# Optimization experiments

Hardware: AMD Instinct MI355X
Metric: run time of the kernel (lower is better)

## Reference

```python
import jax, jax.numpy as jnp
import numpy as np

N = 100000
E = 1600000
R = 4
D_IN = 128
D_H = 128
C = 2


def _rgcn_conv(x, W, src, dst, et):
    """PyG RGCNConv, root_weight=False, bias=False, aggr='mean'.
    x: [N, d_in], W: [R, d_in, d_out]. Per relation: mean over incoming
    edges of that relation of (x[src] @ W_r), summed over relations.
    """
    n, r = x.shape[0], W.shape[0]
    xw = jnp.einsum('ni,rio->rno', x, W)          # [R, N, d_out]
    m = xw[et, src]                               # [E, d_out] per-edge messages
    key = dst * r + et                            # segment per (dst, relation)
    sums = jax.ops.segment_sum(m, key, num_segments=n * r)
    cnt = jax.ops.segment_sum(jnp.ones((m.shape[0],), m.dtype), key, num_segments=n * r)
    mean = sums / jnp.maximum(cnt, 1.0)[:, None]  # [N*R, d_out]
    return mean.reshape(n, r, -1).sum(axis=1)     # sum over relations -> [N, d_out]


def setup_inputs() -> dict:
    key = jax.random.key(0)
    k = jax.random.split(key, 6)
    x = jax.random.normal(k[0], (N, D_IN), dtype=jnp.float32)
    edge_index = jax.random.randint(k[1], (2, E), 0, N, dtype=jnp.int32)
    edge_type = jax.random.randint(k[2], (E,), 0, R, dtype=jnp.int32)
    # Glorot-ish scaled relation weights per layer
    W1 = jax.random.normal(k[3], (R, D_IN, D_H), dtype=jnp.float32) / np.sqrt(D_IN)
    W2 = jax.random.normal(k[4], (R, D_H, D_H), dtype=jnp.float32) / np.sqrt(D_H)
    W3 = jax.random.normal(k[5], (R, D_H, C), dtype=jnp.float32) / np.sqrt(D_H)
    return {"x": x, "edge_index": edge_index, "edge_type": edge_type,
            "W1": W1, "W2": W2, "W3": W3}


def reference(x, edge_index, edge_type, W1, W2, W3):
    src, dst = edge_index[0], edge_index[1]
    # eval mode: dropout is identity
    h = _rgcn_conv(x, W1, src, dst, edge_type)
    h = jnp.tanh(h)
    h = _rgcn_conv(h, W2, src, dst, edge_type)
    h = jnp.tanh(h)
    h = _rgcn_conv(h, W3, src, dst, edge_type)   # [N, C] logits
    return jax.nn.softmax(h, axis=1), h
```

## Files before the change

### kernel.cpp

```cpp
#include <hip/hip_runtime.h>
#include <math.h>

#define N_NODES 100000
#define N_EDGES 1600000
#define RREL 4
#define DDIM 128
#define KDIM 512
#define NKEY 400000

typedef __bf16 bf16x8 __attribute__((ext_vector_type(8)));
typedef float f32x4 __attribute__((ext_vector_type(4)));

__device__ __forceinline__ float bflo(unsigned u){ return __builtin_bit_cast(float, u << 16); }
__device__ __forceinline__ float bfhi(unsigned u){ return __builtin_bit_cast(float, u & 0xffff0000u); }
__device__ __forceinline__ unsigned f2bf(float f){
  unsigned u = __builtin_bit_cast(unsigned, f);
  return (u + 0x7fffu + ((u >> 16) & 1u)) >> 16;
}
__device__ __forceinline__ int iclamp(int v, int lo, int hi){
  return v < lo ? lo : (v > hi ? hi : v);
}


__global__ void hist_kernel(const int* __restrict__ dst, const int* __restrict__ et,
                            int* __restrict__ counts){
  int e = blockIdx.x * 256 + threadIdx.x;
  int key = iclamp(dst[e] * RREL + et[e], 0, NKEY - 1);
  atomicAdd(&counts[key], 1);
}

__global__ void scan_local(const int* __restrict__ in, int* __restrict__ out,
                           int* __restrict__ bsums, int K){
  __shared__ int s[1024];
  int t = threadIdx.x;
  int i = blockIdx.x * 1024 + t;
  int v = (i < K) ? in[i] : 0;
  s[t] = v; __syncthreads();
  for (int off = 1; off < 1024; off <<= 1){
    int x = (t >= off) ? s[t - off] : 0;
    __syncthreads();
    s[t] += x;
    __syncthreads();
  }
  if (i < K) out[i] = s[t] - v;
  if (t == 1023) bsums[blockIdx.x] = s[t];
}

__global__ void scan_sums(int* __restrict__ b, int nb){
  __shared__ int s[1024];
  int t = threadIdx.x;
  int v = (t < nb) ? b[t] : 0;
  s[t] = v; __syncthreads();
  for (int off = 1; off < 1024; off <<= 1){
    int x = (t >= off) ? s[t - off] : 0;
    __syncthreads();
    s[t] += x;
    __syncthreads();
  }
  if (t < nb) b[t] = s[t] - v;
}

__global__ void scan_add(int* __restrict__ out, int* __restrict__ cursor,
                         const int* __restrict__ bsums, int K, int total){
  int t = threadIdx.x;
  int i = blockIdx.x * 1024 + t;
  if (i < K){
    int v = out[i] + bsums[blockIdx.x];
    out[i] = v;
    cursor[i] = v;
  }
  if (i == 0) out[K] = total;
}

__global__ void scatter_kernel(const int* __restrict__ src, const int* __restrict__ dst,
                               const int* __restrict__ et, int* __restrict__ cursor,
                               int* __restrict__ ssrc){
  int e = blockIdx.x * 256 + threadIdx.x;
  int key = iclamp(dst[e] * RREL + et[e], 0, NKEY - 1);
  int p = atomicAdd(&cursor[key], 1);
  p = iclamp(p, 0, N_EDGES - 1);
  ssrc[p] = iclamp(src[e], 0, N_NODES - 1);
}


__global__ void convert_x(const float* __restrict__ x, unsigned* __restrict__ xb){
  int i = blockIdx.x * 256 + threadIdx.x;
  float2 v = *(const float2*)(x + (size_t)i * 2);
  xb[i] = f2bf(v.x) | (f2bf(v.y) << 16);
}


__global__ void transpose_w(const float* __restrict__ W, unsigned short* __restrict__ Bt){
  int idx = blockIdx.x * 256 + threadIdx.x;
  int k = idx >> 7, n = idx & 127;
  Bt[n * KDIM + k] = (unsigned short)f2bf(W[idx]);
}


__global__ __launch_bounds__(256) void fused_layer(const unsigned* __restrict__ hin,
                                                   const int* __restrict__ ssrc,
                                                   const int* __restrict__ offs,
                                                   const __bf16* __restrict__ Bt,
                                                   unsigned short* __restrict__ hout){
  int tid = threadIdx.x;
  int w = tid >> 6, lane = tid & 63;
  int l15 = lane & 15, quad = lane >> 4;
  int n0w = blockIdx.x * 64 + w * 16;
  int n = n0w + l15;
  int valid = (n < N_NODES);

  f32x4 accC[8];
  #pragma unroll
  for (int tc = 0; tc < 8; tc++) accC[tc] = (f32x4){0.f, 0.f, 0.f, 0.f};

  #pragma unroll
  for (int r = 0; r < RREL; r++){
    int ob = valid ? (n * 4 + r) : 0;
    int beg = iclamp(offs[ob], 0, N_EDGES);
    int end = iclamp(offs[ob + 1], beg, N_EDGES);
    if (!valid){ beg = 0; end = 0; }

    float ac[32];
    #pragma unroll
    for (int j = 0; j < 32; j++) ac[j] = 0.f;

    int i = beg;
    int nxt = (i < end) ? ssrc[i] : 0;
    while (i < end){
      int cur = iclamp(nxt, 0, N_NODES - 1);
      i++;
      nxt = (i < end) ? ssrc[i] : 0;
      const uint4* row = (const uint4*)(hin + (size_t)cur * 64 + quad * 4);
      uint4 u0 = row[0];
      uint4 u1 = row[4];
      uint4 u2 = row[8];
      uint4 u3 = row[12];
      ac[ 0] += bflo(u0.x); ac[ 1] += bfhi(u0.x); ac[ 2] += bflo(u0.y); ac[ 3] += bfhi(u0.y);
      ac[ 4] += bflo(u0.z); ac[ 5] += bfhi(u0.z); ac[ 6] += bflo(u0.w); ac[ 7] += bfhi(u0.w);
      ac[ 8] += bflo(u1.x); ac[ 9] += bfhi(u1.x); ac[10] += bflo(u1.y); ac[11] += bfhi(u1.y);
      ac[12] += bflo(u1.z); ac[13] += bfhi(u1.z); ac[14] += bflo(u1.w); ac[15] += bfhi(u1.w);
      ac[16] += bflo(u2.x); ac[17] += bfhi(u2.x); ac[18] += bflo(u2.y); ac[19] += bfhi(u2.y);
      ac[20] += bflo(u2.z); ac[21] += bfhi(u2.z); ac[22] += bflo(u2.w); ac[23] += bfhi(u2.w);
      ac[24] += bflo(u3.x); ac[25] += bfhi(u3.x); ac[26] += bflo(u3.y); ac[27] += bfhi(u3.y);
      ac[28] += bflo(u3.z); ac[29] += bfhi(u3.z); ac[30] += bflo(u3.w); ac[31] += bfhi(u3.w);
    }
    int cnt = end - beg;
    float sc = (cnt > 0) ? 1.0f / (float)cnt : 0.0f;

    #pragma unroll
    for (int s = 0; s < 4; s++){
      uint4 pv;
      pv.x = f2bf(ac[s * 8 + 0] * sc) | (f2bf(ac[s * 8 + 1] * sc) << 16);
      pv.y = f2bf(ac[s * 8 + 2] * sc) | (f2bf(ac[s * 8 + 3] * sc) << 16);
      pv.z = f2bf(ac[s * 8 + 4] * sc) | (f2bf(ac[s * 8 + 5] * sc) << 16);
      pv.w = f2bf(ac[s * 8 + 6] * sc) | (f2bf(ac[s * 8 + 7] * sc) << 16);
      bf16x8 af = __builtin_bit_cast(bf16x8, pv);
      const __bf16* bbase = Bt + r * 128 + s * 32 + quad * 8;
      #pragma unroll
      for (int tc = 0; tc < 8; tc++){
        bf16x8 bfr = *(const bf16x8*)(bbase + (size_t)(tc * 16 + l15) * KDIM);
        accC[tc] = __builtin_amdgcn_mfma_f32_16x16x32_bf16(af, bfr, accC[tc], 0, 0, 0);
      }
    }
  }

  #pragma unroll
  for (int tc = 0; tc < 8; tc++){
    #pragma unroll
    for (int reg = 0; reg < 4; reg++){
      int n2 = n0w + quad * 4 + reg;
      if (n2 < N_NODES){
        float v = tanhf(accC[tc][reg]);
        hout[(size_t)n2 * 128 + tc * 16 + l15] = (unsigned short)f2bf(v);
      }
    }
  }
}


__global__ void compute_z(const unsigned* __restrict__ h2, const float* __restrict__ W3f,
                          float* __restrict__ zt){
  int n = blockIdx.x * 4 + (threadIdx.x >> 6);
  int lane = threadIdx.x & 63;
  unsigned u = h2[(size_t)n * 64 + lane];
  float a = bflo(u), b = bfhi(u);
  float p[8];
  #pragma unroll
  for (int r = 0; r < RREL; r++){
    float4 wv = *(const float4*)(W3f + r * 256 + lane * 4);
    p[r * 2]     = a * wv.x + b * wv.z;
    p[r * 2 + 1] = a * wv.y + b * wv.w;
  }
  #pragma unroll
  for (int m = 32; m >= 1; m >>= 1){
    #pragma unroll
    for (int j = 0; j < 8; j++) p[j] += __shfl_xor(p[j], m);
  }
  if (lane == 0){
    *(float4*)(zt + (size_t)n * 8)     = (float4){p[0], p[1], p[2], p[3]};
    *(float4*)(zt + (size_t)n * 8 + 4) = (float4){p[4], p[5], p[6], p[7]};
  }
}


__global__ void fused_head2(const float* __restrict__ zt,
                            const int* __restrict__ ssrc,
                            const int* __restrict__ offs,
                            float* __restrict__ out){
  int k = blockIdx.x * 256 + threadIdx.x;
  if (k >= NKEY) return;
  int r = k & 3;
  int beg = iclamp(offs[k], 0, N_EDGES);
  int end = iclamp(offs[k + 1], beg, N_EDGES);
  float a0 = 0.f, a1 = 0.f, b0 = 0.f, b1 = 0.f, c0 = 0.f, c1 = 0.f, d0 = 0.f, d1 = 0.f;
  int i = beg;
  for (; i + 4 <= end; i += 4){
    int s0 = iclamp(ssrc[i],     0, N_NODES - 1);
    int s1 = iclamp(ssrc[i + 1], 0, N_NODES - 1);
    int s2 = iclamp(ssrc[i + 2], 0, N_NODES - 1);
    int s3 = iclamp(ssrc[i + 3], 0, N_NODES - 1);
    float2 v0 = *(const float2*)(zt + (size_t)s0 * 8 + r * 2);
    float2 v1 = *(const float2*)(zt + (size_t)s1 * 8 + r * 2);
    float2 v2 = *(const float2*)(zt + (size_t)s2 * 8 + r * 2);
    float2 v3 = *(const float2*)(zt + (size_t)s3 * 8 + r * 2);
    a0 += v0.x; a1 += v0.y;
    b0 += v1.x; b1 += v1.y;
    c0 += v2.x; c1 += v2.y;
    d0 += v3.x; d1 += v3.y;
  }
  for (; i < end; i++){
    int s = iclamp(ssrc[i], 0, N_NODES - 1);
    float2 v = *(const float2*)(zt + (size_t)s * 8 + r * 2);
    a0 += v.x; a1 += v.y;
  }
  int cnt = end - beg;
  float sc = (cnt > 0) ? 1.0f / (float)cnt : 0.0f;
  float dA = (a0 + b0 + c0 + d0) * sc;
  float dB = (a1 + b1 + c1 + d1) * sc;
  dA += __shfl_xor(dA, 1); dB += __shfl_xor(dB, 1);
  dA += __shfl_xor(dA, 2); dB += __shfl_xor(dB, 2);
  if (r == 0){
    int n = k >> 2;
    float mx = fmaxf(dA, dB);
    float e0 = __expf(dA - mx), e1 = __expf(dB - mx);
    float inv = 1.0f / (e0 + e1);
    *(float2*)(out + 2 * n) = (float2){e0 * inv, e1 * inv};
    *(float2*)(out + 2 * N_NODES + 2 * n) = (float2){dA, dB};
  }
}


extern "C" void kernel_launch(void* const* d_in, const int* in_sizes, int n_in,
                              void* d_out, int out_size, void* d_ws, size_t ws_size,
                              hipStream_t stream){
  const float* x  = (const float*)d_in[0];
  const int* ei   = (const int*)d_in[1];
  const int* et   = (const int*)d_in[2];
  const float* W1 = (const float*)d_in[3];
  const float* W2 = (const float*)d_in[4];
  const float* W3 = (const float*)d_in[5];
  float* out = (float*)d_out;
  const int* src = ei;
  const int* dst = ei + N_EDGES;

  char* p = (char*)d_ws;
  auto alloc = [&](size_t bytes) -> char* {
    char* q = p; p += (bytes + 63) & ~(size_t)63; return q;
  };
  int* counts = (int*)alloc((size_t)NKEY * 4);
  int* cursor = counts;
  int* offs   = (int*)alloc((size_t)(NKEY + 1) * 4);
  int* bsums  = (int*)alloc(1024 * 4);
  int* ssrc   = (int*)alloc((size_t)N_EDGES * 4);
  unsigned short* Bt = (unsigned short*)alloc((size_t)DDIM * KDIM * 2);
  unsigned short* h1 = (unsigned short*)alloc((size_t)N_NODES * DDIM * 2);
  unsigned short* h2 = (unsigned short*)alloc((size_t)N_NODES * DDIM * 2);
  unsigned* xb = (unsigned*)h2;
  float* zt = (float*)h1;

  hipMemsetAsync(counts, 0, (size_t)NKEY * 4, stream);
  hist_kernel<<<N_EDGES / 256, 256, 0, stream>>>(dst, et, counts);
  int nb = (NKEY + 1023) / 1024;
  scan_local<<<nb, 1024, 0, stream>>>(counts, offs, bsums, NKEY);
  scan_sums<<<1, 1024, 0, stream>>>(bsums, nb);
  scan_add<<<nb, 1024, 0, stream>>>(offs, cursor, bsums, NKEY, N_EDGES);
  scatter_kernel<<<N_EDGES / 256, 256, 0, stream>>>(src, dst, et, cursor, ssrc);

  int fgrid = (N_NODES + 63) / 64;

  convert_x<<<(N_NODES * 64) / 256, 256, 0, stream>>>(x, xb);
  transpose_w<<<(DDIM * KDIM) / 256, 256, 0, stream>>>(W1, Bt);
  fused_layer<<<fgrid, 256, 0, stream>>>(xb, ssrc, offs, (const __bf16*)Bt, h1);
  transpose_w<<<(DDIM * KDIM) / 256, 256, 0, stream>>>(W2, Bt);
  fused_layer<<<fgrid, 256, 0, stream>>>((const unsigned*)h1, ssrc, offs, (const __bf16*)Bt, h2);
  compute_z<<<N_NODES / 4, 256, 0, stream>>>((const unsigned*)h2, W3, zt);
  fused_head2<<<(NKEY + 255) / 256, 256, 0, stream>>>(zt, ssrc, offs, out);
}
```

Measured before the change: 753.9 us.

## Reorder CSR keys relation-major and aggregate per block with LDS atomics

Changes the segment key layout from dst*R+rel to rel*N+dst, so each block's 64 destination nodes for one relation form a contiguous edge range. The low 6 bits of the destination are packed into the upper bits of each sorted source index. The fused layer now walks that edge range wave-cooperatively, with each lane loading one bf16 pair per edge and accumulating into a shared-memory tile through float atomics. The aim is to remove per-node load imbalance and serial per-thread edge loops, at the cost of LDS atomic contention, extra barriers and per-relation LDS zeroing.

```diff
diff --git a/kernel.cpp b/kernel.cpp
--- a/kernel.cpp
+++ b/kernel.cpp
@@ -7,6 +7,7 @@
 #define DDIM 128
 #define KDIM 512
 #define NKEY 400000
+#define SRCMASK 0x03FFFFFFu
 
 typedef __bf16 bf16x8 __attribute__((ext_vector_type(8)));
 typedef float f32x4 __attribute__((ext_vector_type(4)));
@@ -25,8 +26,9 @@
 __global__ void hist_kernel(const int* __restrict__ dst, const int* __restrict__ et,
                             int* __restrict__ counts){
   int e = blockIdx.x * 256 + threadIdx.x;
-  int key = iclamp(dst[e] * RREL + et[e], 0, NKEY - 1);
-  atomicAdd(&counts[key], 1);
+  int d = iclamp(dst[e], 0, N_NODES - 1);
+  int t = iclamp(et[e], 0, RREL - 1);
+  atomicAdd(&counts[t * N_NODES + d], 1);
 }
 
 __global__ void scan_local(const int* __restrict__ in, int* __restrict__ out,
@@ -74,12 +76,14 @@
 
 __global__ void scatter_kernel(const int* __restrict__ src, const int* __restrict__ dst,
                                const int* __restrict__ et, int* __restrict__ cursor,
-                               int* __restrict__ ssrc){
+                               unsigned* __restrict__ ssrc){
   int e = blockIdx.x * 256 + threadIdx.x;
-  int key = iclamp(dst[e] * RREL + et[e], 0, NKEY - 1);
+  int d = iclamp(dst[e], 0, N_NODES - 1);
+  int t = iclamp(et[e], 0, RREL - 1);
+  int key = t * N_NODES + d;
   int p = atomicAdd(&cursor[key], 1);
   p = iclamp(p, 0, N_EDGES - 1);
-  ssrc[p] = iclamp(src[e], 0, N_NODES - 1);
+  ssrc[p] = (unsigned)iclamp(src[e], 0, N_NODES - 1) | ((unsigned)(d & 63) << 26);
 }
 
 
@@ -98,62 +102,75 @@
 
 
 __global__ __launch_bounds__(256) void fused_layer(const unsigned* __restrict__ hin,
-                                                   const int* __restrict__ ssrc,
+                                                   const unsigned* __restrict__ ssrc,
                                                    const int* __restrict__ offs,
                                                    const __bf16* __restrict__ Bt,
                                                    unsigned short* __restrict__ hout){
+  __shared__ float agg[64][132];
+
   int tid = threadIdx.x;
   int w = tid >> 6, lane = tid & 63;
   int l15 = lane & 15, quad = lane >> 4;
-  int n0w = blockIdx.x * 64 + w * 16;
-  int n = n0w + l15;
-  int valid = (n < N_NODES);
+  int n0 = blockIdx.x * 64;
+  int nn = (N_NODES - n0 < 64) ? (N_NODES - n0) : 64;
+  int n0w = n0 + w * 16;
 
   f32x4 accC[8];
   #pragma unroll
   for (int tc = 0; tc < 8; tc++) accC[tc] = (f32x4){0.f, 0.f, 0.f, 0.f};
 
-  #pragma unroll
+  float* af_ = &agg[0][0];
+
   for (int r = 0; r < RREL; r++){
-    int ob = valid ? (n * 4 + r) : 0;
-    int beg = iclamp(offs[ob], 0, N_EDGES);
-    int end = iclamp(offs[ob + 1], beg, N_EDGES);
-    if (!valid){ beg = 0; end = 0; }
-
-    float ac[32];
-    #pragma unroll
-    for (int j = 0; j < 32; j++) ac[j] = 0.f;
-
-    int i = beg;
-    int nxt = (i < end) ? ssrc[i] : 0;
-    while (i < end){
-      int cur = iclamp(nxt, 0, N_NODES - 1);
-      i++;
-      nxt = (i < end) ? ssrc[i] : 0;
-      const uint4* row = (const uint4*)(hin + (size_t)cur * 64 + quad * 4);
-      uint4 u0 = row[0];
-      uint4 u1 = row[4];
-      uint4 u2 = row[8];
-      uint4 u3 = row[12];
-      ac[ 0] += bflo(u0.x); ac[ 1] += bfhi(u0.x); ac[ 2] += bflo(u0.y); ac[ 3] += bfhi(u0.y);
-      ac[ 4] += bflo(u0.z); ac[ 5] += bfhi(u0.z); ac[ 6] += bflo(u0.w); ac[ 7] += bfhi(u0.w);
-      ac[ 8] += bflo(u1.x); ac[ 9] += bfhi(u1.x); ac[10] += bflo(u1.y); ac[11] += bfhi(u1.y);
-      ac[12] += bflo(u1.z); ac[13] += bfhi(u1.z); ac[14] += bflo(u1.w); ac[15] += bfhi(u1.w);
-      ac[16] += bflo(u2.x); ac[17] += bfhi(u2.x); ac[18] += bflo(u2.y); ac[19] += bfhi(u2.y);
-      ac[20] += bflo(u2.z); ac[21] += bfhi(u2.z); ac[22] += bflo(u2.w); ac[23] += bfhi(u2.w);
-      ac[24] += bflo(u3.x); ac[25] += bfhi(u3.x); ac[26] += bflo(u3.y); ac[27] += bfhi(u3.y);
-      ac[28] += bflo(u3.z); ac[29] += bfhi(u3.z); ac[30] += bflo(u3.w); ac[31] += bfhi(u3.w);
+    __syncthreads();
+    for (int idx = tid; idx < 64 * 132; idx += 256) af_[idx] = 0.f;
+    __syncthreads();
+
+    int kbase = r * N_NODES + n0;
+    int ebeg = offs[kbase];
+    int eend = offs[kbase + nn];
+    int e = ebeg + w;
+    for (; e + 12 < eend; e += 16){
+      int eu = __builtin_amdgcn_readfirstlane(e);
+      unsigned w0 = ssrc[eu], w1 = ssrc[eu + 4], w2 = ssrc[eu + 8], w3 = ssrc[eu + 12];
+      unsigned q0 = hin[(size_t)(w0 & SRCMASK) * 64 + lane];
+      unsigned q1 = hin[(size_t)(w1 & SRCMASK) * 64 + lane];
+      unsigned q2 = hin[(size_t)(w2 & SRCMASK) * 64 + lane];
+      unsigned q3 = hin[(size_t)(w3 & SRCMASK) * 64 + lane];
+      atomicAdd(&agg[w0 >> 26][2 * lane],     bflo(q0));
+      atomicAdd(&agg[w0 >> 26][2 * lane + 1], bfhi(q0));
+      atomicAdd(&agg[w1 >> 26][2 * lane],     bflo(q1));
+      atomicAdd(&agg[w1 >> 26][2 * lane + 1], bfhi(q1));
+      atomicAdd(&agg[w2 >> 26][2 * lane],     bflo(q2));
+      atomicAdd(&agg[w2 >> 26][2 * lane + 1], bfhi(q2));
+      atomicAdd(&agg[w3 >> 26][2 * lane],     bflo(q3));
+      atomicAdd(&agg[w3 >> 26][2 * lane + 1], bfhi(q3));
     }
-    int cnt = end - beg;
-    float sc = (cnt > 0) ? 1.0f / (float)cnt : 0.0f;
+    for (; e < eend; e += 4){
+      int eu = __builtin_amdgcn_readfirstlane(e);
+      unsigned w0 = ssrc[eu];
+      unsigned q0 = hin[(size_t)(w0 & SRCMASK) * 64 + lane];
+      atomicAdd(&agg[w0 >> 26][2 * lane],     bflo(q0));
+      atomicAdd(&agg[w0 >> 26][2 * lane + 1], bfhi(q0));
+    }
+    __syncthreads();
+
+    int lnm = w * 16 + l15;
+    int n2 = n0 + lnm;
+    int ob = r * N_NODES + iclamp(n2, 0, N_NODES - 1);
+    int cb = offs[ob], ce = offs[ob + 1];
+    int cnt = ce - cb;
+    float sc = (cnt > 0 && n2 < N_NODES) ? 1.0f / (float)cnt : 0.0f;
 
     #pragma unroll
     for (int s = 0; s < 4; s++){
+      const float4* ap = (const float4*)&agg[lnm][s * 32 + quad * 8];
+      float4 x0 = ap[0], x1 = ap[1];
       uint4 pv;
-      pv.x = f2bf(ac[s * 8 + 0] * sc) | (f2bf(ac[s * 8 + 1] * sc) << 16);
-      pv.y = f2bf(ac[s * 8 + 2] * sc) | (f2bf(ac[s * 8 + 3] * sc) << 16);
-      pv.z = f2bf(ac[s * 8 + 4] * sc) | (f2bf(ac[s * 8 + 5] * sc) << 16);
-      pv.w = f2bf(ac[s * 8 + 6] * sc) | (f2bf(ac[s * 8 + 7] * sc) << 16);
+      pv.x = f2bf(x0.x * sc) | (f2bf(x0.y * sc) << 16);
+      pv.y = f2bf(x0.z * sc) | (f2bf(x0.w * sc) << 16);
+      pv.z = f2bf(x1.x * sc) | (f2bf(x1.y * sc) << 16);
+      pv.w = f2bf(x1.z * sc) | (f2bf(x1.w * sc) << 16);
       bf16x8 af = __builtin_bit_cast(bf16x8, pv);
       const __bf16* bbase = Bt + r * 128 + s * 32 + quad * 8;
       #pragma unroll
@@ -204,21 +221,22 @@
 
 
 __global__ void fused_head2(const float* __restrict__ zt,
-                            const int* __restrict__ ssrc,
+                            const unsigned* __restrict__ ssrc,
                             const int* __restrict__ offs,
                             float* __restrict__ out){
-  int k = blockIdx.x * 256 + threadIdx.x;
-  if (k >= NKEY) return;
-  int r = k & 3;
-  int beg = iclamp(offs[k], 0, N_EDGES);
-  int end = iclamp(offs[k + 1], beg, N_EDGES);
+  int t = blockIdx.x * 256 + threadIdx.x;
+  if (t >= NKEY) return;
+  int n = t >> 2, r = t & 3;
+  int k2 = r * N_NODES + n;
+  int beg = iclamp(offs[k2], 0, N_EDGES);
+  int end = iclamp(offs[k2 + 1], beg, N_EDGES);
   float a0 = 0.f, a1 = 0.f, b0 = 0.f, b1 = 0.f, c0 = 0.f, c1 = 0.f, d0 = 0.f, d1 = 0.f;
   int i = beg;
   for (; i + 4 <= end; i += 4){
-    int s0 = iclamp(ssrc[i],     0, N_NODES - 1);
-    int s1 = iclamp(ssrc[i + 1], 0, N_NODES - 1);
-    int s2 = iclamp(ssrc[i + 2], 0, N_NODES - 1);
-    int s3 = iclamp(ssrc[i + 3], 0, N_NODES - 1);
+    int s0 = (int)(ssrc[i]     & SRCMASK);
+    int s1 = (int)(ssrc[i + 1] & SRCMASK);
+    int s2 = (int)(ssrc[i + 2] & SRCMASK);
+    int s3 = (int)(ssrc[i + 3] & SRCMASK);
     float2 v0 = *(const float2*)(zt + (size_t)s0 * 8 + r * 2);
     float2 v1 = *(const float2*)(zt + (size_t)s1 * 8 + r * 2);
     float2 v2 = *(const float2*)(zt + (size_t)s2 * 8 + r * 2);
@@ -229,7 +247,7 @@
     d0 += v3.x; d1 += v3.y;
   }
   for (; i < end; i++){
-    int s = iclamp(ssrc[i], 0, N_NODES - 1);
+    int s = (int)(ssrc[i] & SRCMASK);
     float2 v = *(const float2*)(zt + (size_t)s * 8 + r * 2);
     a0 += v.x; a1 += v.y;
   }
@@ -240,7 +258,6 @@
   dA += __shfl_xor(dA, 1); dB += __shfl_xor(dB, 1);
   dA += __shfl_xor(dA, 2); dB += __shfl_xor(dB, 2);
   if (r == 0){
-    int n = k >> 2;
     float mx = fmaxf(dA, dB);
     float e0 = __expf(dA - mx), e1 = __expf(dB - mx);
     float inv = 1.0f / (e0 + e1);
@@ -271,7 +288,7 @@
   int* cursor = counts;
   int* offs   = (int*)alloc((size_t)(NKEY + 1) * 4);
   int* bsums  = (int*)alloc(1024 * 4);
-  int* ssrc   = (int*)alloc((size_t)N_EDGES * 4);
+  unsigned* ssrc = (unsigned*)alloc((size_t)N_EDGES * 4);
   unsigned short* Bt = (unsigned short*)alloc((size_t)DDIM * KDIM * 2);
   unsigned short* h1 = (unsigned short*)alloc((size_t)N_NODES * DDIM * 2);
   unsigned short* h2 = (unsigned short*)alloc((size_t)N_NODES * DDIM * 2);
```

New measurement: 2.774 ms. +268.0%, slower.

## Double-buffer neighbor row gathers via global_load_lds with swizzled LDS layout

Applied to the files above, without the earlier changes.

Replaces the per-lane serial gather loop in fused_layer with a wave-cooperative scheme. Each wave runs the maximum degree among its 16 nodes. On every step the 64 lanes issue direct global-to-LDS 16-byte loads for the next neighbor row of each of the 16 nodes into a double buffer, while the current buffer is read back with an XOR swizzle to avoid bank conflicts. Nodes that have run out of edges load from a zero row. The goal is to coalesce accesses and overlap gather latency with accumulation, at the cost of wasted iterations when degrees within a wave are uneven, plus extra LDS use.

```diff
diff --git a/kernel.cpp b/kernel.cpp
--- a/kernel.cpp
+++ b/kernel.cpp
@@ -20,6 +20,10 @@
 __device__ __forceinline__ int iclamp(int v, int lo, int hi){
   return v < lo ? lo : (v > hi ? hi : v);
 }
+
+#define GLL(gp, lp) __builtin_amdgcn_global_load_lds( \
+    (const __attribute__((address_space(1))) void*)(gp), \
+    (__attribute__((address_space(3))) void*)(lp), 16, 0, 0)
 
 
 __global__ void hist_kernel(const int* __restrict__ dst, const int* __restrict__ et,
@@ -101,17 +105,27 @@
                                                    const int* __restrict__ ssrc,
                                                    const int* __restrict__ offs,
                                                    const __bf16* __restrict__ Bt,
+                                                   const char* __restrict__ zrow,
                                                    unsigned short* __restrict__ hout){
+  __shared__ uint4 smem4[2048];
+
   int tid = threadIdx.x;
   int w = tid >> 6, lane = tid & 63;
   int l15 = lane & 15, quad = lane >> 4;
   int n0w = blockIdx.x * 64 + w * 16;
   int n = n0w + l15;
   int valid = (n < N_NODES);
+  const char* hinB = (const char*)hin;
+  uint4* lw = &smem4[w << 9];
 
   f32x4 accC[8];
   #pragma unroll
   for (int tc = 0; tc < 8; tc++) accC[tc] = (f32x4){0.f, 0.f, 0.f, 0.f};
+
+  int q0 = (l15 ^ (quad)) * 16;
+  int q1 = (l15 ^ (4 + quad)) * 16;
+  int q2 = (l15 ^ (8 + quad)) * 16;
+  int q3 = (l15 ^ (12 + quad)) * 16;
 
   #pragma unroll
   for (int r = 0; r < RREL; r++){
@@ -119,33 +133,79 @@
     int beg = iclamp(offs[ob], 0, N_EDGES);
     int end = iclamp(offs[ob + 1], beg, N_EDGES);
     if (!valid){ beg = 0; end = 0; }
+    int deg = end - beg;
+
+    int trip = deg;
+    #pragma unroll
+    for (int k = 1; k < 64; k <<= 1){
+      int o = __shfl_xor(trip, k);
+      trip = trip > o ? trip : o;
+    }
 
     float ac[32];
     #pragma unroll
     for (int j = 0; j < 32; j++) ac[j] = 0.f;
 
-    int i = beg;
-    int nxt = (i < end) ? ssrc[i] : 0;
-    while (i < end){
-      int cur = iclamp(nxt, 0, N_NODES - 1);
-      i++;
-      nxt = (i < end) ? ssrc[i] : 0;
-      const uint4* row = (const uint4*)(hin + (size_t)cur * 64 + quad * 4);
-      uint4 u0 = row[0];
-      uint4 u1 = row[4];
-      uint4 u2 = row[8];
-      uint4 u3 = row[12];
-      ac[ 0] += bflo(u0.x); ac[ 1] += bfhi(u0.x); ac[ 2] += bflo(u0.y); ac[ 3] += bfhi(u0.y);
-      ac[ 4] += bflo(u0.z); ac[ 5] += bfhi(u0.z); ac[ 6] += bflo(u0.w); ac[ 7] += bfhi(u0.w);
-      ac[ 8] += bflo(u1.x); ac[ 9] += bfhi(u1.x); ac[10] += bflo(u1.y); ac[11] += bfhi(u1.y);
-      ac[12] += bflo(u1.z); ac[13] += bfhi(u1.z); ac[14] += bflo(u1.w); ac[15] += bfhi(u1.w);
-      ac[16] += bflo(u2.x); ac[17] += bfhi(u2.x); ac[18] += bflo(u2.y); ac[19] += bfhi(u2.y);
-      ac[20] += bflo(u2.z); ac[21] += bfhi(u2.z); ac[22] += bflo(u2.w); ac[23] += bfhi(u2.w);
-      ac[24] += bflo(u3.x); ac[25] += bfhi(u3.x); ac[26] += bflo(u3.y); ac[27] += bfhi(u3.y);
-      ac[28] += bflo(u3.z); ac[29] += bfhi(u3.z); ac[30] += bflo(u3.w); ac[31] += bfhi(u3.w);
+    if (trip > 0){
+      int bg0 = __shfl(beg, quad),      eg0 = __shfl(end, quad);
+      int bg1 = __shfl(beg, 4 + quad),  eg1 = __shfl(end, 4 + quad);
+      int bg2 = __shfl(beg, 8 + quad),  eg2 = __shfl(end, 8 + quad);
+      int bg3 = __shfl(beg, 12 + quad), eg3 = __shfl(end, 12 + quad);
+
+      int sv0 = ssrc[iclamp(bg0, 0, N_EDGES - 1)];
+      int sv1 = ssrc[iclamp(bg1, 0, N_EDGES - 1)];
+      int sv2 = ssrc[iclamp(bg2, 0, N_EDGES - 1)];
+      int sv3 = ssrc[iclamp(bg3, 0, N_EDGES - 1)];
+      {
+        const char* a0 = (0 < eg0 - bg0) ? hinB + (size_t)(unsigned)sv0 * 256 + q0 : zrow + q0;
+        const char* a1 = (0 < eg1 - bg1) ? hinB + (size_t)(unsigned)sv1 * 256 + q1 : zrow + q1;
+        const char* a2 = (0 < eg2 - bg2) ? hinB + (size_t)(unsigned)sv2 * 256 + q2 : zrow + q2;
+        const char* a3 = (0 < eg3 - bg3) ? hinB + (size_t)(unsigned)sv3 * 256 + q3 : zrow + q3;
+        GLL(a0, lw + 0);
+        GLL(a1, lw + 64);
+        GLL(a2, lw + 128);
+        GLL(a3, lw + 192);
+      }
+
+      for (int i = 0; i < trip; i++){
+        int b = i & 1;
+        if (i + 1 < trip){
+          sv0 = ssrc[iclamp(bg0 + i + 1, 0, N_EDGES - 1)];
+          sv1 = ssrc[iclamp(bg1 + i + 1, 0, N_EDGES - 1)];
+          sv2 = ssrc[iclamp(bg2 + i + 1, 0, N_EDGES - 1)];
+          sv3 = ssrc[iclamp(bg3 + i + 1, 0, N_EDGES - 1)];
+          uint4* db = lw + ((b ^ 1) << 8);
+          const char* a0 = (i + 1 < eg0 - bg0) ? hinB + (size_t)(unsigned)sv0 * 256 + q0 : zrow + q0;
+          const char* a1 = (i + 1 < eg1 - bg1) ? hinB + (size_t)(unsigned)sv1 * 256 + q1 : zrow + q1;
+          const char* a2 = (i + 1 < eg2 - bg2) ? hinB + (size_t)(unsigned)sv2 * 256 + q2 : zrow + q2;
+          const char* a3 = (i + 1 < eg3 - bg3) ? hinB + (size_t)(unsigned)sv3 * 256 + q3 : zrow + q3;
+          GLL(a0, db + 0);
+          GLL(a1, db + 64);
+          GLL(a2, db + 128);
+          GLL(a3, db + 192);
+          asm volatile("s_waitcnt vmcnt(4)" ::: "memory");
+        } else {
+          asm volatile("s_waitcnt vmcnt(0)" ::: "memory");
+        }
+        __builtin_amdgcn_sched_barrier(0);
+
+        const uint4* rb = lw + (b << 8) + (l15 << 4);
+        uint4 u0 = rb[(0 * 4 + quad) ^ l15];
+        uint4 u1 = rb[(1 * 4 + quad) ^ l15];
+        uint4 u2 = rb[(2 * 4 + quad) ^ l15];
+        uint4 u3 = rb[(3 * 4 + quad) ^ l15];
+        ac[ 0] += bflo(u0.x); ac[ 1] += bfhi(u0.x); ac[ 2] += bflo(u0.y); ac[ 3] += bfhi(u0.y);
+        ac[ 4] += bflo(u0.z); ac[ 5] += bfhi(u0.z); ac[ 6] += bflo(u0.w); ac[ 7] += bfhi(u0.w);
+        ac[ 8] += bflo(u1.x); ac[ 9] += bfhi(u1.x); ac[10] += bflo(u1.y); ac[11] += bfhi(u1.y);
+        ac[12] += bflo(u1.z); ac[13] += bfhi(u1.z); ac[14] += bflo(u1.w); ac[15] += bfhi(u1.w);
+        ac[16] += bflo(u2.x); ac[17] += bfhi(u2.x); ac[18] += bflo(u2.y); ac[19] += bfhi(u2.y);
+        ac[20] += bflo(u2.z); ac[21] += bfhi(u2.z); ac[22] += bflo(u2.w); ac[23] += bfhi(u2.w);
+        ac[24] += bflo(u3.x); ac[25] += bfhi(u3.x); ac[26] += bflo(u3.y); ac[27] += bfhi(u3.y);
+        ac[28] += bflo(u3.z); ac[29] += bfhi(u3.z); ac[30] += bflo(u3.w); ac[31] += bfhi(u3.w);
+      }
     }
-    int cnt = end - beg;
-    float sc = (cnt > 0) ? 1.0f / (float)cnt : 0.0f;
+
+    float sc = (deg > 0) ? 1.0f / (float)deg : 0.0f;
 
     #pragma unroll
     for (int s = 0; s < 4; s++){
@@ -272,6 +332,7 @@
   int* offs   = (int*)alloc((size_t)(NKEY + 1) * 4);
   int* bsums  = (int*)alloc(1024 * 4);
   int* ssrc   = (int*)alloc((size_t)N_EDGES * 4);
+  char* zrow  = alloc(256);
   unsigned short* Bt = (unsigned short*)alloc((size_t)DDIM * KDIM * 2);
   unsigned short* h1 = (unsigned short*)alloc((size_t)N_NODES * DDIM * 2);
   unsigned short* h2 = (unsigned short*)alloc((size_t)N_NODES * DDIM * 2);
@@ -279,6 +340,7 @@
   float* zt = (float*)h1;
 
   hipMemsetAsync(counts, 0, (size_t)NKEY * 4, stream);
+  hipMemsetAsync(zrow, 0, 256, stream);
   hist_kernel<<<N_EDGES / 256, 256, 0, stream>>>(dst, et, counts);
   int nb = (NKEY + 1023) / 1024;
   scan_local<<<nb, 1024, 0, stream>>>(counts, offs, bsums, NKEY);
@@ -290,9 +352,9 @@
 
   convert_x<<<(N_NODES * 64) / 256, 256, 0, stream>>>(x, xb);
   transpose_w<<<(DDIM * KDIM) / 256, 256, 0, stream>>>(W1, Bt);
-  fused_layer<<<fgrid, 256, 0, stream>>>(xb, ssrc, offs, (const __bf16*)Bt, h1);
+  fused_layer<<<fgrid, 256, 0, stream>>>(xb, ssrc, offs, (const __bf16*)Bt, zrow, h1);
   transpose_w<<<(DDIM * KDIM) / 256, 256, 0, stream>>>(W2, Bt);
-  fused_layer<<<fgrid, 256, 0, stream>>>((const unsigned*)h1, ssrc, offs, (const __bf16*)Bt, h2);
+  fused_layer<<<fgrid, 256, 0, stream>>>((const unsigned*)h1, ssrc, offs, (const __bf16*)Bt, zrow, h2);
   compute_z<<<N_NODES / 4, 256, 0, stream>>>((const unsigned*)h2, W3, zt);
   fused_head2<<<(NKEY + 255) / 256, 256, 0, stream>>>(zt, ssrc, offs, out);
 }
```

Result: slower. 798.3 us (+5.9%).
